# Optimization experiments

Measured on AMD Instinct MI355X. Metric: run time of the kernel, lower is better.

The kernel has to match this reference:

```python
import jax, jax.numpy as jnp
import numpy as np

N_NODES = 50000
N_REL = 8
IN_DIM = 128
HID = 128
N_EDGES = 800000
N_TRIP = 100000


def setup_inputs() -> dict:
    key = jax.random.key(0)
    ks = jax.random.split(key, 12)
    s = 0.05
    return {
        "emb": jax.random.normal(ks[0], (N_NODES, IN_DIM), jnp.float32),
        "W0": jax.random.normal(ks[1], (N_REL, IN_DIM, HID), jnp.float32) * s,
        "root0": jax.random.normal(ks[2], (IN_DIM, HID), jnp.float32) * s,
        "b0": jnp.zeros((HID,), jnp.float32),
        "W1": jax.random.normal(ks[3], (N_REL, HID, HID), jnp.float32) * s,
        "root1": jax.random.normal(ks[4], (HID, HID), jnp.float32) * s,
        "b1": jnp.zeros((HID,), jnp.float32),
        "rel_emb": jax.random.normal(ks[5], (N_REL, HID), jnp.float32),
        "edge_index": jax.random.randint(ks[6], (2, N_EDGES), 0, N_NODES, jnp.int64 if jax.config.read('jax_enable_x64') else jnp.int32),
        "edge_type": jax.random.randint(ks[7], (N_EDGES,), 0, N_REL, jnp.int32),
        "head_idx": jax.random.randint(ks[8], (N_TRIP,), 0, N_NODES, jnp.int32),
        "rel_idx": jax.random.randint(ks[9], (N_TRIP,), 0, N_REL, jnp.int32),
        "tail_idx": jax.random.randint(ks[10], (N_TRIP,), 0, N_NODES, jnp.int32),
    }


def _rgcn_layer(h, W, root, bias, src, dst, edge_type):
    # PyG RGCNConv: per-relation MEAN aggregation of neighbor features at dst,
    # transformed by the relation weight, plus root transform and bias.
    # Mean commutes with the linear map, so aggregate raw features first.
    n, r = N_NODES, N_REL
    seg = dst * r + edge_type  # (E,) joint (dst, relation) segment id
    msg = h[src]               # (E, d) irregular gather
    sums = jax.ops.segment_sum(msg, seg, num_segments=n * r)          # (N*R, d)
    cnt = jax.ops.segment_sum(jnp.ones((src.shape[0],), h.dtype), seg,
                              num_segments=n * r)                     # (N*R,)
    mean = (sums / jnp.maximum(cnt, 1.0)[:, None]).reshape(n, r, -1)  # (N, R, d)
    return jnp.einsum('nrd,rdh->nh', mean, W) + h @ root + bias


def reference(emb, W0, root0, b0, W1, root1, b1, rel_emb,
              edge_index, edge_type, head_idx, rel_idx, tail_idx):
    src = edge_index[0]
    dst = edge_index[1]
    et = edge_type.astype(jnp.int32)
    h = emb
    h = jax.nn.relu(_rgcn_layer(h, W0, root0, b0, src, dst, et))
    h = jax.nn.relu(_rgcn_layer(h, W1, root1, b1, src, dst, et))
    # DistMult score: sum(h_head * r * h_tail)
    score = jnp.sum(h[head_idx] * rel_emb[rel_idx] * h[tail_idx], axis=-1)
    return score
```

## Files before the change

kernel.cpp:

```cpp
#include <hip/hip_runtime.h>
#include <hip/hip_bf16.h>

#define N_NODES 50000
#define N_REL   8
#define DIM     128
#define N_EDGES 800000
#define N_TRIP  100000
#define NSEG    (N_NODES * N_REL)
#define NBUCKET 196
#define CAP     6144
#define CPAD    132

typedef __attribute__((ext_vector_type(8))) short bf16x8;
typedef __attribute__((ext_vector_type(4))) float f32x4;

static __device__ __forceinline__ unsigned short f2b(float f) {
    __hip_bfloat16 h = __float2bfloat16(f);
    return *reinterpret_cast<unsigned short*>(&h);
}
static __device__ __forceinline__ float blo(unsigned int u) {
    return __uint_as_float(u << 16);
}
static __device__ __forceinline__ float bhi(unsigned int u) {
    return __uint_as_float(u & 0xffff0000u);
}
static __device__ __forceinline__ int lds_off(int row, int chunk) {
    return (row * 16 + (chunk ^ (row & 7))) * 8;
}

__global__ __launch_bounds__(256) void bucket_scatter(
        const int* __restrict__ edge_index,
        const int* __restrict__ edge_type,
        int* __restrict__ gcnt,
        unsigned int* __restrict__ slack) {
    __shared__ int hist[NBUCKET];
    __shared__ int cur[NBUCKET];
    int tid = threadIdx.x;
    for (int i = tid; i < NBUCKET; i += 256) hist[i] = 0;
    __syncthreads();
    int base = blockIdx.x * 4096;
    unsigned int w[16];
    int bk[16];
    #pragma unroll
    for (int i = 0; i < 16; ++i) {
        int e = base + i * 256 + tid;
        if (e < N_EDGES) {
            int src = edge_index[e];
            int dst = edge_index[N_EDGES + e];
            int r = edge_type[e];
            w[i] = (unsigned int)src | ((unsigned int)r << 16) |
                   ((unsigned int)(dst & 255) << 19);
            bk[i] = dst >> 8;
            atomicAdd(&hist[bk[i]], 1);
        } else {
            bk[i] = -1;
        }
    }
    __syncthreads();
    for (int i = tid; i < NBUCKET; i += 256)
        cur[i] = atomicAdd(&gcnt[i], hist[i]);
    __syncthreads();
    #pragma unroll
    for (int i = 0; i < 16; ++i) {
        if (bk[i] >= 0) {
            int p = atomicAdd(&cur[bk[i]], 1);
            if (p < CAP) slack[(size_t)bk[i] * CAP + p] = w[i];
        }
    }
}

__global__ void bucket_scan(const int* __restrict__ gcnt,
                            int* __restrict__ gbase,
                            int* __restrict__ offsets) {
    __shared__ int sh[256];
    int t = threadIdx.x;
    int v = (t < NBUCKET) ? gcnt[t] : 0;
    sh[t] = v;
    __syncthreads();
    #pragma unroll
    for (int off = 1; off < 256; off <<= 1) {
        int x = (t >= off) ? sh[t - off] : 0;
        __syncthreads();
        sh[t] += x;
        __syncthreads();
    }
    if (t < NBUCKET) gbase[t] = sh[t] - v;
    if (t == 0) offsets[NSEG] = N_EDGES;
}

__global__ __launch_bounds__(256) void bucket_sort(
        const unsigned int* __restrict__ slack,
        const int* __restrict__ gcnt,
        const int* __restrict__ gbase,
        unsigned int* __restrict__ sorted_pack,
        int* __restrict__ offsets,
        float* __restrict__ invcnt) {
    __shared__ unsigned int ebuf[CAP];
    __shared__ unsigned int obuf[CAP];
    __shared__ int hist[2048];
    __shared__ int excl[2048];
    __shared__ int sh[256];
    int b = blockIdx.x, t = threadIdx.x;
    int n = gcnt[b]; if (n > CAP) n = CAP;
    int bb = gbase[b];
    for (int i = t; i < n; i += 256) ebuf[i] = slack[(size_t)b * CAP + i];
    for (int i = t; i < 2048; i += 256) hist[i] = 0;
    __syncthreads();
    for (int i = t; i < n; i += 256) {
        unsigned int w = ebuf[i];
        int seg = (int)((w >> 19) << 3) | (int)((w >> 16) & 7u);
        atomicAdd(&hist[seg], 1);
    }
    __syncthreads();
    int c[8];
    int s = 0;
    #pragma unroll
    for (int j = 0; j < 8; ++j) { c[j] = hist[t * 8 + j]; s += c[j]; }
    sh[t] = s;
    __syncthreads();
    #pragma unroll
    for (int off = 1; off < 256; off <<= 1) {
        int x = (t >= off) ? sh[t - off] : 0;
        __syncthreads();
        sh[t] += x;
        __syncthreads();
    }
    int ex = sh[t] - s;
    #pragma unroll
    for (int j = 0; j < 8; ++j) { excl[t * 8 + j] = ex; ex += c[j]; }
    __syncthreads();
    #pragma unroll
    for (int j = 0; j < 8; ++j) hist[t * 8 + j] = excl[t * 8 + j];
    __syncthreads();
    for (int i = t; i < n; i += 256) {
        unsigned int w = ebuf[i];
        int seg = (int)((w >> 19) << 3) | (int)((w >> 16) & 7u);
        int p = atomicAdd(&hist[seg], 1);
        obuf[p] = w & 0x7ffffu;
    }
    __syncthreads();
    for (int i = t; i < n; i += 256) sorted_pack[bb + i] = obuf[i];
    int segbase = b * 2048;
    #pragma unroll
    for (int j = 0; j < 8; ++j) {
        int gseg = segbase + t * 8 + j;
        if (gseg < NSEG) {
            offsets[gseg] = bb + excl[t * 8 + j];
            invcnt[gseg] = (c[j] > 0) ? 1.0f / (float)c[j] : 0.f;
        }
    }
}

__global__ void cvt_emb_kernel(const float* __restrict__ src,
                               unsigned short* __restrict__ dst) {
    int i = blockIdx.x * blockDim.x + threadIdx.x;
    const int npair = N_NODES * DIM / 2;
    if (i >= npair) return;
    float2 v = ((const float2*)src)[i];
    unsigned int p = (unsigned int)f2b(v.x) | ((unsigned int)f2b(v.y) << 16);
    ((unsigned int*)dst)[i] = p;
}

__global__ void cvt_w2_kernel(const float* __restrict__ root0,
                              const float* __restrict__ W0,
                              const float* __restrict__ root1,
                              const float* __restrict__ W1,
                              unsigned short* __restrict__ Wt2a,
                              unsigned short* __restrict__ Wt2b) {
    int s = blockIdx.x;
    int n = blockIdx.y;
    int k = threadIdx.x;
    const float* root = blockIdx.z ? root1 : root0;
    const float* W    = blockIdx.z ? W1 : W0;
    unsigned short* Wt2 = blockIdx.z ? Wt2b : Wt2a;
    float v = (s == 0) ? root[k * 128 + n]
                       : W[((size_t)(s - 1) * 128 + k) * 128 + n];
    Wt2[((size_t)s * 128 + n) * 128 + k] = f2b(v);
}

__global__ __launch_bounds__(256) void gemm9_all(
        const unsigned short* __restrict__ hb,
        const unsigned short* __restrict__ Wt2,
        unsigned short* __restrict__ Y) {
    __shared__ unsigned short Bs[128 * 16 * 8];
    __shared__ unsigned short Cs[64 * CPAD];

    int tid = threadIdx.x;
    int wave = tid >> 6, lane = tid & 63;
    int wm = wave & 1, wn = wave >> 1;
    int quad = lane >> 4, l16 = lane & 15;
    int row0 = blockIdx.x * 64;

    bf16x8 afr[2][4];
    #pragma unroll
    for (int i = 0; i < 2; ++i) {
        int grow = row0 + wm * 32 + i * 16 + l16;
        if (grow >= N_NODES) grow = N_NODES - 1;
        #pragma unroll
        for (int kk = 0; kk < 4; ++kk)
            afr[i][kk] = *(const bf16x8*)(hb + (size_t)grow * DIM + kk * 32 + quad * 8);
    }

    int er = tid >> 2, ec = (tid & 3) * 32;
    int egrow = row0 + er;
    bool estore = (egrow < N_NODES);

    for (int s = 0; s < 9; ++s) {
        __syncthreads();
        {
            int n = tid >> 1, c0 = (tid & 1) * 8;
            const unsigned short* gp = Wt2 + ((size_t)s * 128 + n) * 128 + c0 * 8;
            #pragma unroll
            for (int q = 0; q < 8; ++q)
                *(bf16x8*)&Bs[lds_off(n, c0 + q)] = *(const bf16x8*)(gp + q * 8);
        }
        __syncthreads();

        f32x4 acc[2][4];
        #pragma unroll
        for (int i = 0; i < 2; ++i)
            #pragma unroll
            for (int j = 0; j < 4; ++j) acc[i][j] = (f32x4){0.f, 0.f, 0.f, 0.f};

        #pragma unroll
        for (int kk = 0; kk < 4; ++kk) {
            int chunk = kk * 4 + quad;
            bf16x8 bfr[4];
            #pragma unroll
            for (int j = 0; j < 4; ++j)
                bfr[j] = *(const bf16x8*)&Bs[lds_off(wn * 64 + j * 16 + l16, chunk)];
            #pragma unroll
            for (int i = 0; i < 2; ++i)
                #pragma unroll
                for (int j = 0; j < 4; ++j)
                    acc[i][j] = __builtin_amdgcn_mfma_f32_16x16x32_bf16(
                        afr[i][kk], bfr[j], acc[i][j], 0, 0, 0);
        }

        #pragma unroll
        for (int i = 0; i < 2; ++i) {
            int rb = wm * 32 + i * 16 + quad * 4;
            #pragma unroll
            for (int j = 0; j < 4; ++j) {
                int col = wn * 64 + j * 16 + l16;
                #pragma unroll
                for (int r = 0; r < 4; ++r)
                    Cs[(rb + r) * CPAD + col] = f2b(acc[i][j][r]);
            }
        }
        __syncthreads();
        if (estore) {
            const uint4* cp = (const uint4*)&Cs[er * CPAD + ec];
            uint4* yp = (uint4*)(Y + ((size_t)s * N_NODES + egrow) * 128 + ec);
            uint4 v0 = cp[0], v1 = cp[1], v2 = cp[2], v3 = cp[3];
            yp[0] = v0; yp[1] = v1; yp[2] = v2; yp[3] = v3;
        }
    }
}

__global__ __launch_bounds__(256) void aggregate_out(
        const unsigned short* __restrict__ Y,
        const float* __restrict__ bias,
        const int* __restrict__ offsets,
        const unsigned int* __restrict__ sorted_pack,
        const float* __restrict__ invcnt,
        unsigned short* __restrict__ hout) {
    int dst = blockIdx.x * 4 + (threadIdx.x >> 6);
    if (dst >= N_NODES) return;
    int lane = threadIdx.x & 63;
    const unsigned int* Yu = (const unsigned int*)Y;

    unsigned int r0 = Yu[(size_t)dst * 64 + lane];
    float a0 = blo(r0), a1 = bhi(r0);

    int beg = offsets[dst * N_REL];
    int end = offsets[dst * N_REL + N_REL];
    for (int base = beg; base < end; base += 64) {
        int np = end - base; if (np > 64) np = 64;
        unsigned int pk = 0; float ivl = 0.f;
        if (lane < np) {
            pk = sorted_pack[base + lane];
            ivl = invcnt[dst * N_REL + (int)(pk >> 16)];
        }
        int j = 0;
        for (; j + 3 < np; j += 4) {
            unsigned int p0 = __shfl((int)pk, j, 64);
            unsigned int p1 = __shfl((int)pk, j + 1, 64);
            unsigned int p2 = __shfl((int)pk, j + 2, 64);
            unsigned int p3 = __shfl((int)pk, j + 3, 64);
            float i0 = __shfl(ivl, j, 64);
            float i1 = __shfl(ivl, j + 1, 64);
            float i2 = __shfl(ivl, j + 2, 64);
            float i3 = __shfl(ivl, j + 3, 64);
            unsigned int v0 = Yu[((size_t)(1 + (p0 >> 16)) * N_NODES + (p0 & 0xffffu)) * 64 + lane];
            unsigned int v1 = Yu[((size_t)(1 + (p1 >> 16)) * N_NODES + (p1 & 0xffffu)) * 64 + lane];
            unsigned int v2 = Yu[((size_t)(1 + (p2 >> 16)) * N_NODES + (p2 & 0xffffu)) * 64 + lane];
            unsigned int v3 = Yu[((size_t)(1 + (p3 >> 16)) * N_NODES + (p3 & 0xffffu)) * 64 + lane];
            a0 = fmaf(blo(v0), i0, a0); a1 = fmaf(bhi(v0), i0, a1);
            a0 = fmaf(blo(v1), i1, a0); a1 = fmaf(bhi(v1), i1, a1);
            a0 = fmaf(blo(v2), i2, a0); a1 = fmaf(bhi(v2), i2, a1);
            a0 = fmaf(blo(v3), i3, a0); a1 = fmaf(bhi(v3), i3, a1);
        }
        for (; j < np; ++j) {
            unsigned int pj = __shfl((int)pk, j, 64);
            float ij = __shfl(ivl, j, 64);
            unsigned int v = Yu[((size_t)(1 + (pj >> 16)) * N_NODES + (pj & 0xffffu)) * 64 + lane];
            a0 = fmaf(blo(v), ij, a0); a1 = fmaf(bhi(v), ij, a1);
        }
    }
    float2 bv = ((const float2*)bias)[lane];
    a0 = fmaxf(a0 + bv.x, 0.f);
    a1 = fmaxf(a1 + bv.y, 0.f);
    unsigned int po = (unsigned int)f2b(a0) | ((unsigned int)f2b(a1) << 16);
    ((unsigned int*)(hout + (size_t)dst * DIM))[lane] = po;
}

__global__ void score_kernel(const unsigned short* __restrict__ hb,
                             const float* __restrict__ rel_emb,
                             const int* __restrict__ head,
                             const int* __restrict__ rel,
                             const int* __restrict__ tail,
                             float* __restrict__ out) {
    int t = blockIdx.x * 4 + (threadIdx.x >> 6);
    if (t >= N_TRIP) return;
    int lane = threadIdx.x & 63;
    unsigned int ph = ((const unsigned int*)(hb + (size_t)head[t] * DIM))[lane];
    unsigned int pt = ((const unsigned int*)(hb + (size_t)tail[t] * DIM))[lane];
    float2 rr = ((const float2*)(rel_emb + (size_t)rel[t] * DIM))[lane];
    float s = blo(ph) * rr.x * blo(pt) + bhi(ph) * rr.y * bhi(pt);
    #pragma unroll
    for (int off = 32; off; off >>= 1) s += __shfl_xor(s, off, 64);
    if (lane == 0) out[t] = s;
}

extern "C" void kernel_launch(void* const* d_in, const int* in_sizes, int n_in,
                              void* d_out, int out_size, void* d_ws, size_t ws_size,
                              hipStream_t stream) {
    const float* emb     = (const float*)d_in[0];
    const float* W0      = (const float*)d_in[1];
    const float* root0   = (const float*)d_in[2];
    const float* b0      = (const float*)d_in[3];
    const float* W1      = (const float*)d_in[4];
    const float* root1   = (const float*)d_in[5];
    const float* b1      = (const float*)d_in[6];
    const float* rel_emb = (const float*)d_in[7];
    const int* edge_index = (const int*)d_in[8];
    const int* edge_type  = (const int*)d_in[9];
    const int* head_idx   = (const int*)d_in[10];
    const int* rel_idx    = (const int*)d_in[11];
    const int* tail_idx   = (const int*)d_in[12];
    float* out = (float*)d_out;

    char* p = (char*)d_ws;
    size_t y_bytes   = (size_t)9 * N_NODES * DIM * sizeof(unsigned short);
    size_t hb_bytes  = (size_t)N_NODES * DIM * sizeof(unsigned short);
    size_t wt2_bytes = (size_t)9 * 128 * 128 * sizeof(unsigned short);
    unsigned short* Y    = (unsigned short*)p; p += y_bytes;
    unsigned short* embb = (unsigned short*)p; p += hb_bytes;
    unsigned short* h1b  = (unsigned short*)p; p += hb_bytes;
    unsigned short* h2b  = (unsigned short*)p; p += hb_bytes;
    unsigned short* Wt2a = (unsigned short*)p; p += wt2_bytes;
    unsigned short* Wt2b = (unsigned short*)p; p += wt2_bytes;
    int* offsets = (int*)p;           p += (size_t)(NSEG + 1) * sizeof(int);
    float* invcnt = (float*)p;        p += (size_t)NSEG * sizeof(float);
    unsigned int* sorted_pack = (unsigned int*)p; p += (size_t)N_EDGES * sizeof(unsigned int);
    unsigned int* slack = (unsigned int*)p; p += (size_t)NBUCKET * CAP * sizeof(unsigned int);
    int* gcnt  = (int*)p;             p += (size_t)NBUCKET * sizeof(int);
    int* gbase = (int*)p;
    (void)ws_size; (void)in_sizes; (void)n_in; (void)out_size;

    dim3 blk256(256);

    hipMemsetAsync(gcnt, 0, (size_t)NBUCKET * sizeof(int), stream);
    bucket_scatter<<<(N_EDGES + 4095) / 4096, blk256, 0, stream>>>(edge_index, edge_type,
                                                                   gcnt, slack);
    bucket_scan<<<1, 256, 0, stream>>>(gcnt, gbase, offsets);
    bucket_sort<<<NBUCKET, blk256, 0, stream>>>(slack, gcnt, gbase, sorted_pack,
                                                offsets, invcnt);

    cvt_emb_kernel<<<(N_NODES * DIM / 2 + 255) / 256, blk256, 0, stream>>>(emb, embb);
    cvt_w2_kernel<<<dim3(9, 128, 2), 128, 0, stream>>>(root0, W0, root1, W1, Wt2a, Wt2b);

    int ggrid = (N_NODES + 63) / 64;
    int agrid = (N_NODES + 3) / 4;

    gemm9_all<<<ggrid, blk256, 0, stream>>>(embb, Wt2a, Y);
    aggregate_out<<<agrid, blk256, 0, stream>>>(Y, b0, offsets, sorted_pack, invcnt, h1b);

    gemm9_all<<<ggrid, blk256, 0, stream>>>(h1b, Wt2b, Y);
    aggregate_out<<<agrid, blk256, 0, stream>>>(Y, b1, offsets, sorted_pack, invcnt, h2b);

    score_kernel<<<(N_TRIP + 3) / 4, blk256, 0, stream>>>(h2b, rel_emb, head_idx, rel_idx,
                                                          tail_idx, out);
}
```

Measured before the change: 365.9 us.

## Remove LDS staging and barriers from per-relation GEMM, load weights directly

Rewrites the 9-slice GEMM so each wave owns 16 rows and loops over all 128 output columns. B fragments now come straight from global memory (L2-resident weights) instead of being staged through swizzled LDS. Results are stored directly as scattered 2-byte writes instead of through an LDS transpose with coalesced 16-byte stores. This removes all __syncthreads and LDS use. The cost is more global load traffic for weights and poorly coalesced output stores.

```diff
diff --git a/kernel.cpp b/kernel.cpp
--- a/kernel.cpp
+++ b/kernel.cpp
@@ -9,7 +9,6 @@
 #define NSEG    (N_NODES * N_REL)
 #define NBUCKET 196
 #define CAP     6144
-#define CPAD    132
 
 typedef __attribute__((ext_vector_type(8))) short bf16x8;
 typedef __attribute__((ext_vector_type(4))) float f32x4;
@@ -23,9 +22,6 @@
 }
 static __device__ __forceinline__ float bhi(unsigned int u) {
     return __uint_as_float(u & 0xffff0000u);
-}
-static __device__ __forceinline__ int lds_off(int row, int chunk) {
-    return (row * 16 + (chunk ^ (row & 7))) * 8;
 }
 
 __global__ __launch_bounds__(256) void bucket_scatter(
@@ -178,82 +174,48 @@
     Wt2[((size_t)s * 128 + n) * 128 + k] = f2b(v);
 }
 
-__global__ __launch_bounds__(256) void gemm9_all(
+__global__ __launch_bounds__(256) void gemm9_nobar(
         const unsigned short* __restrict__ hb,
         const unsigned short* __restrict__ Wt2,
         unsigned short* __restrict__ Y) {
-    __shared__ unsigned short Bs[128 * 16 * 8];
-    __shared__ unsigned short Cs[64 * CPAD];
-
     int tid = threadIdx.x;
     int wave = tid >> 6, lane = tid & 63;
-    int wm = wave & 1, wn = wave >> 1;
     int quad = lane >> 4, l16 = lane & 15;
-    int row0 = blockIdx.x * 64;
-
-    bf16x8 afr[2][4];
-    #pragma unroll
-    for (int i = 0; i < 2; ++i) {
-        int grow = row0 + wm * 32 + i * 16 + l16;
+    int row0 = blockIdx.x * 64 + wave * 16;
+
+    bf16x8 afr[4];
+    {
+        int grow = row0 + l16;
         if (grow >= N_NODES) grow = N_NODES - 1;
+        const unsigned short* gp = hb + (size_t)grow * DIM;
         #pragma unroll
         for (int kk = 0; kk < 4; ++kk)
-            afr[i][kk] = *(const bf16x8*)(hb + (size_t)grow * DIM + kk * 32 + quad * 8);
-    }
-
-    int er = tid >> 2, ec = (tid & 3) * 32;
-    int egrow = row0 + er;
-    bool estore = (egrow < N_NODES);
-
+            afr[kk] = *(const bf16x8*)(gp + kk * 32 + quad * 8);
+    }
+
+    int srow0 = row0 + quad * 4;
     for (int s = 0; s < 9; ++s) {
-        __syncthreads();
-        {
-            int n = tid >> 1, c0 = (tid & 1) * 8;
-            const unsigned short* gp = Wt2 + ((size_t)s * 128 + n) * 128 + c0 * 8;
-            #pragma unroll
-            for (int q = 0; q < 8; ++q)
-                *(bf16x8*)&Bs[lds_off(n, c0 + q)] = *(const bf16x8*)(gp + q * 8);
-        }
-        __syncthreads();
-
-        f32x4 acc[2][4];
+        const unsigned short* Ws = Wt2 + (size_t)s * 128 * 128;
+        unsigned short* Ys = Y + (size_t)s * N_NODES * 128;
         #pragma unroll
-        for (int i = 0; i < 2; ++i)
-            #pragma unroll
-            for (int j = 0; j < 4; ++j) acc[i][j] = (f32x4){0.f, 0.f, 0.f, 0.f};
-
-        #pragma unroll
-        for (int kk = 0; kk < 4; ++kk) {
-            int chunk = kk * 4 + quad;
+        for (int j = 0; j < 8; ++j) {
+            const unsigned short* bp = Ws + (size_t)(j * 16 + l16) * 128;
             bf16x8 bfr[4];
             #pragma unroll
-            for (int j = 0; j < 4; ++j)
-                bfr[j] = *(const bf16x8*)&Bs[lds_off(wn * 64 + j * 16 + l16, chunk)];
+            for (int kk = 0; kk < 4; ++kk)
+                bfr[kk] = *(const bf16x8*)(bp + kk * 32 + quad * 8);
+            f32x4 acc = (f32x4){0.f, 0.f, 0.f, 0.f};
             #pragma unroll
-            for (int i = 0; i < 2; ++i)
-                #pragma unroll
-                for (int j = 0; j < 4; ++j)
-                    acc[i][j] = __builtin_amdgcn_mfma_f32_16x16x32_bf16(
-                        afr[i][kk], bfr[j], acc[i][j], 0, 0, 0);
-        }
-
-        #pragma unroll
-        for (int i = 0; i < 2; ++i) {
-            int rb = wm * 32 + i * 16 + quad * 4;
+            for (int kk = 0; kk < 4; ++kk)
+                acc = __builtin_amdgcn_mfma_f32_16x16x32_bf16(
+                    afr[kk], bfr[kk], acc, 0, 0, 0);
+            int gc = j * 16 + l16;
             #pragma unroll
-            for (int j = 0; j < 4; ++j) {
-                int col = wn * 64 + j * 16 + l16;
-                #pragma unroll
-                for (int r = 0; r < 4; ++r)
-                    Cs[(rb + r) * CPAD + col] = f2b(acc[i][j][r]);
+            for (int r = 0; r < 4; ++r) {
+                int gr = srow0 + r;
+                if (gr < N_NODES)
+                    Ys[(size_t)gr * 128 + gc] = f2b(acc[r]);
             }
-        }
-        __syncthreads();
-        if (estore) {
-            const uint4* cp = (const uint4*)&Cs[er * CPAD + ec];
-            uint4* yp = (uint4*)(Y + ((size_t)s * N_NODES + egrow) * 128 + ec);
-            uint4 v0 = cp[0], v1 = cp[1], v2 = cp[2], v3 = cp[3];
-            yp[0] = v0; yp[1] = v1; yp[2] = v2; yp[3] = v3;
         }
     }
 }
@@ -384,10 +346,10 @@
     int ggrid = (N_NODES + 63) / 64;
     int agrid = (N_NODES + 3) / 4;
 
-    gemm9_all<<<ggrid, blk256, 0, stream>>>(embb, Wt2a, Y);
+    gemm9_nobar<<<ggrid, blk256, 0, stream>>>(embb, Wt2a, Y);
     aggregate_out<<<agrid, blk256, 0, stream>>>(Y, b0, offsets, sorted_pack, invcnt, h1b);
 
-    gemm9_all<<<ggrid, blk256, 0, stream>>>(h1b, Wt2b, Y);
+    gemm9_nobar<<<ggrid, blk256, 0, stream>>>(h1b, Wt2b, Y);
     aggregate_out<<<agrid, blk256, 0, stream>>>(Y, b1, offsets, sorted_pack, invcnt, h2b);
 
     score_kernel<<<(N_TRIP + 3) / 4, blk256, 0, stream>>>(h2b, rel_emb, head_idx, rel_idx,
```

After: 505.3 us. 1.38x slower.

## Load GEMM B fragments directly to registers and use per-wave epilogue staging

Applied to the files above, without the earlier changes.

The 9-slice GEMM no longer stages each weight slice in shared memory. Each wave now loads its B fragments straight from global memory (L2-resident weights) into registers. The output epilogue uses a private per-wave LDS tile instead of a block-wide tile, so all __syncthreads barriers are removed from the slice loop. This trades block barriers and LDS traffic for redundant global loads of the weights across waves, plus higher register pressure from holding 16 B fragments.

```diff
diff --git a/kernel.cpp b/kernel.cpp
--- a/kernel.cpp
+++ b/kernel.cpp
@@ -9,7 +9,7 @@
 #define NSEG    (N_NODES * N_REL)
 #define NBUCKET 196
 #define CAP     6144
-#define CPAD    132
+#define CROWS   72
 
 typedef __attribute__((ext_vector_type(8))) short bf16x8;
 typedef __attribute__((ext_vector_type(4))) float f32x4;
@@ -23,9 +23,6 @@
 }
 static __device__ __forceinline__ float bhi(unsigned int u) {
     return __uint_as_float(u & 0xffff0000u);
-}
-static __device__ __forceinline__ int lds_off(int row, int chunk) {
-    return (row * 16 + (chunk ^ (row & 7))) * 8;
 }
 
 __global__ __launch_bounds__(256) void bucket_scatter(
@@ -178,12 +175,11 @@
     Wt2[((size_t)s * 128 + n) * 128 + k] = f2b(v);
 }
 
-__global__ __launch_bounds__(256) void gemm9_all(
+__global__ __launch_bounds__(256) void gemm9_reg(
         const unsigned short* __restrict__ hb,
         const unsigned short* __restrict__ Wt2,
         unsigned short* __restrict__ Y) {
-    __shared__ unsigned short Bs[128 * 16 * 8];
-    __shared__ unsigned short Cs[64 * CPAD];
+    __shared__ unsigned short Cs[4][32 * CROWS];
 
     int tid = threadIdx.x;
     int wave = tid >> 6, lane = tid & 63;
@@ -201,20 +197,21 @@
             afr[i][kk] = *(const bf16x8*)(hb + (size_t)grow * DIM + kk * 32 + quad * 8);
     }
 
-    int er = tid >> 2, ec = (tid & 3) * 32;
-    int egrow = row0 + er;
-    bool estore = (egrow < N_NODES);
+    unsigned short* cw = &Cs[wave][0];
+    int rrow = lane >> 3, rch = lane & 7;
 
     for (int s = 0; s < 9; ++s) {
-        __syncthreads();
-        {
-            int n = tid >> 1, c0 = (tid & 1) * 8;
-            const unsigned short* gp = Wt2 + ((size_t)s * 128 + n) * 128 + c0 * 8;
+        const unsigned short* Ws = Wt2 + (size_t)s * 128 * 128;
+        unsigned short* Ys = Y + (size_t)s * N_NODES * 128;
+
+        bf16x8 bfr[4][4];
+        #pragma unroll
+        for (int j = 0; j < 4; ++j) {
+            const unsigned short* bp = Ws + (size_t)(wn * 64 + j * 16 + l16) * 128;
             #pragma unroll
-            for (int q = 0; q < 8; ++q)
-                *(bf16x8*)&Bs[lds_off(n, c0 + q)] = *(const bf16x8*)(gp + q * 8);
-        }
-        __syncthreads();
+            for (int kk = 0; kk < 4; ++kk)
+                bfr[j][kk] = *(const bf16x8*)(bp + kk * 32 + quad * 8);
+        }
 
         f32x4 acc[2][4];
         #pragma unroll
@@ -223,38 +220,33 @@
             for (int j = 0; j < 4; ++j) acc[i][j] = (f32x4){0.f, 0.f, 0.f, 0.f};
 
         #pragma unroll
-        for (int kk = 0; kk < 4; ++kk) {
-            int chunk = kk * 4 + quad;
-            bf16x8 bfr[4];
-            #pragma unroll
-            for (int j = 0; j < 4; ++j)
-                bfr[j] = *(const bf16x8*)&Bs[lds_off(wn * 64 + j * 16 + l16, chunk)];
+        for (int kk = 0; kk < 4; ++kk)
             #pragma unroll
             for (int i = 0; i < 2; ++i)
                 #pragma unroll
                 for (int j = 0; j < 4; ++j)
                     acc[i][j] = __builtin_amdgcn_mfma_f32_16x16x32_bf16(
-                        afr[i][kk], bfr[j], acc[i][j], 0, 0, 0);
-        }
-
-        #pragma unroll
-        for (int i = 0; i < 2; ++i) {
-            int rb = wm * 32 + i * 16 + quad * 4;
+                        afr[i][kk], bfr[j][kk], acc[i][j], 0, 0, 0);
+
+        #pragma unroll
+        for (int i = 0; i < 2; ++i)
             #pragma unroll
-            for (int j = 0; j < 4; ++j) {
-                int col = wn * 64 + j * 16 + l16;
+            for (int j = 0; j < 4; ++j)
                 #pragma unroll
                 for (int r = 0; r < 4; ++r)
-                    Cs[(rb + r) * CPAD + col] = f2b(acc[i][j][r]);
-            }
-        }
-        __syncthreads();
-        if (estore) {
-            const uint4* cp = (const uint4*)&Cs[er * CPAD + ec];
-            uint4* yp = (uint4*)(Y + ((size_t)s * N_NODES + egrow) * 128 + ec);
-            uint4 v0 = cp[0], v1 = cp[1], v2 = cp[2], v3 = cp[3];
-            yp[0] = v0; yp[1] = v1; yp[2] = v2; yp[3] = v3;
-        }
+                    cw[(i * 16 + quad * 4 + r) * CROWS + j * 16 + l16] =
+                        f2b(acc[i][j][r]);
+        asm volatile("" ::: "memory");
+
+        #pragma unroll
+        for (int t = 0; t < 4; ++t) {
+            int lr = t * 8 + rrow;
+            int grow = row0 + wm * 32 + lr;
+            uint4 v = *(const uint4*)&cw[lr * CROWS + rch * 8];
+            if (grow < N_NODES)
+                *(uint4*)(Ys + (size_t)grow * 128 + wn * 64 + rch * 8) = v;
+        }
+        asm volatile("" ::: "memory");
     }
 }
 
@@ -384,10 +376,10 @@
     int ggrid = (N_NODES + 63) / 64;
     int agrid = (N_NODES + 3) / 4;
 
-    gemm9_all<<<ggrid, blk256, 0, stream>>>(embb, Wt2a, Y);
+    gemm9_reg<<<ggrid, blk256, 0, stream>>>(embb, Wt2a, Y);
     aggregate_out<<<agrid, blk256, 0, stream>>>(Y, b0, offsets, sorted_pack, invcnt, h1b);
 
-    gemm9_all<<<ggrid, blk256, 0, stream>>>(h1b, Wt2b, Y);
+    gemm9_reg<<<ggrid, blk256, 0, stream>>>(h1b, Wt2b, Y);
     aggregate_out<<<agrid, blk256, 0, stream>>>(Y, b1, offsets, sorted_pack, invcnt, h2b);
 
     score_kernel<<<(N_TRIP + 3) / 4, blk256, 0, stream>>>(h2b, rel_emb, head_idx, rel_idx,
```

Result: slower. 376.3 us (+2.8%).

## Split GEMM columns across two blocks, store directly, and unroll gather by eight

Applied to the files above, without the earlier changes.

The 9-way GEMM now splits the 128 output columns into two 64-column tiles across a second grid dimension. This halves the LDS weight tile and per-wave accumulators, which should raise occupancy and parallelism. The LDS staging of the output tile is removed, so results go straight to global memory as scattered 2-byte stores, and one barrier per slice is dropped at the cost of less coalesced writes. Each column block also reloads the A fragments. Separately, the aggregation gather loop is unrolled from 4 to 8 edges so more loads are in flight.

```diff
diff --git a/kernel.cpp b/kernel.cpp
--- a/kernel.cpp
+++ b/kernel.cpp
@@ -9,7 +9,6 @@
 #define NSEG    (N_NODES * N_REL)
 #define NBUCKET 196
 #define CAP     6144
-#define CPAD    132
 
 typedef __attribute__((ext_vector_type(8))) short bf16x8;
 typedef __attribute__((ext_vector_type(4))) float f32x4;
@@ -178,18 +177,18 @@
     Wt2[((size_t)s * 128 + n) * 128 + k] = f2b(v);
 }
 
-__global__ __launch_bounds__(256) void gemm9_all(
+__global__ __launch_bounds__(256) void gemm9_bn64(
         const unsigned short* __restrict__ hb,
         const unsigned short* __restrict__ Wt2,
         unsigned short* __restrict__ Y) {
-    __shared__ unsigned short Bs[128 * 16 * 8];
-    __shared__ unsigned short Cs[64 * CPAD];
+    __shared__ unsigned short Bs[64 * 16 * 8];
 
     int tid = threadIdx.x;
     int wave = tid >> 6, lane = tid & 63;
     int wm = wave & 1, wn = wave >> 1;
     int quad = lane >> 4, l16 = lane & 15;
     int row0 = blockIdx.x * 64;
+    int col0 = blockIdx.y * 64;
 
     bf16x8 afr[2][4];
     #pragma unroll
@@ -201,59 +200,52 @@
             afr[i][kk] = *(const bf16x8*)(hb + (size_t)grow * DIM + kk * 32 + quad * 8);
     }
 
-    int er = tid >> 2, ec = (tid & 3) * 32;
-    int egrow = row0 + er;
-    bool estore = (egrow < N_NODES);
-
     for (int s = 0; s < 9; ++s) {
         __syncthreads();
         {
-            int n = tid >> 1, c0 = (tid & 1) * 8;
-            const unsigned short* gp = Wt2 + ((size_t)s * 128 + n) * 128 + c0 * 8;
-            #pragma unroll
-            for (int q = 0; q < 8; ++q)
+            int n = tid >> 2, c0 = (tid & 3) * 4;
+            const unsigned short* gp = Wt2 + ((size_t)s * 128 + col0 + n) * 128 + c0 * 8;
+            #pragma unroll
+            for (int q = 0; q < 4; ++q)
                 *(bf16x8*)&Bs[lds_off(n, c0 + q)] = *(const bf16x8*)(gp + q * 8);
         }
         __syncthreads();
 
-        f32x4 acc[2][4];
+        f32x4 acc[2][2];
         #pragma unroll
         for (int i = 0; i < 2; ++i)
             #pragma unroll
-            for (int j = 0; j < 4; ++j) acc[i][j] = (f32x4){0.f, 0.f, 0.f, 0.f};
+            for (int j = 0; j < 2; ++j) acc[i][j] = (f32x4){0.f, 0.f, 0.f, 0.f};
 
         #pragma unroll
         for (int kk = 0; kk < 4; ++kk) {
             int chunk = kk * 4 + quad;
-            bf16x8 bfr[4];
-            #pragma unroll
-            for (int j = 0; j < 4; ++j)
-                bfr[j] = *(const bf16x8*)&Bs[lds_off(wn * 64 + j * 16 + l16, chunk)];
+            bf16x8 bfr[2];
+            #pragma unroll
+            for (int j = 0; j < 2; ++j)
+                bfr[j] = *(const bf16x8*)&Bs[lds_off(wn * 32 + j * 16 + l16, chunk)];
             #pragma unroll
             for (int i = 0; i < 2; ++i)
                 #pragma unroll
-                for (int j = 0; j < 4; ++j)
+                for (int j = 0; j < 2; ++j)
                     acc[i][j] = __builtin_amdgcn_mfma_f32_16x16x32_bf16(
                         afr[i][kk], bfr[j], acc[i][j], 0, 0, 0);
         }
 
+        unsigned short* Ys = Y + (size_t)s * N_NODES * 128;
         #pragma unroll
         for (int i = 0; i < 2; ++i) {
-            int rb = wm * 32 + i * 16 + quad * 4;
-            #pragma unroll
-            for (int j = 0; j < 4; ++j) {
-                int col = wn * 64 + j * 16 + l16;
+            int gr0 = row0 + wm * 32 + i * 16 + quad * 4;
+            #pragma unroll
+            for (int j = 0; j < 2; ++j) {
+                int gc = col0 + wn * 32 + j * 16 + l16;
                 #pragma unroll
-                for (int r = 0; r < 4; ++r)
-                    Cs[(rb + r) * CPAD + col] = f2b(acc[i][j][r]);
+                for (int r = 0; r < 4; ++r) {
+                    int grow = gr0 + r;
+                    if (grow < N_NODES)
+                        Ys[(size_t)grow * 128 + gc] = f2b(acc[i][j][r]);
+                }
             }
-        }
-        __syncthreads();
-        if (estore) {
-            const uint4* cp = (const uint4*)&Cs[er * CPAD + ec];
-            uint4* yp = (uint4*)(Y + ((size_t)s * N_NODES + egrow) * 128 + ec);
-            uint4 v0 = cp[0], v1 = cp[1], v2 = cp[2], v3 = cp[3];
-            yp[0] = v0; yp[1] = v1; yp[2] = v2; yp[3] = v3;
         }
     }
 }
@@ -283,23 +275,22 @@
             ivl = invcnt[dst * N_REL + (int)(pk >> 16)];
         }
         int j = 0;
-        for (; j + 3 < np; j += 4) {
-            unsigned int p0 = __shfl((int)pk, j, 64);
-            unsigned int p1 = __shfl((int)pk, j + 1, 64);
-            unsigned int p2 = __shfl((int)pk, j + 2, 64);
-            unsigned int p3 = __shfl((int)pk, j + 3, 64);
-            float i0 = __shfl(ivl, j, 64);
-            float i1 = __shfl(ivl, j + 1, 64);
-            float i2 = __shfl(ivl, j + 2, 64);
-            float i3 = __shfl(ivl, j + 3, 64);
-            unsigned int v0 = Yu[((size_t)(1 + (p0 >> 16)) * N_NODES + (p0 & 0xffffu)) * 64 + lane];
-            unsigned int v1 = Yu[((size_t)(1 + (p1 >> 16)) * N_NODES + (p1 & 0xffffu)) * 64 + lane];
-            unsigned int v2 = Yu[((size_t)(1 + (p2 >> 16)) * N_NODES + (p2 & 0xffffu)) * 64 + lane];
-            unsigned int v3 = Yu[((size_t)(1 + (p3 >> 16)) * N_NODES + (p3 & 0xffffu)) * 64 + lane];
-            a0 = fmaf(blo(v0), i0, a0); a1 = fmaf(bhi(v0), i0, a1);
-            a0 = fmaf(blo(v1), i1, a0); a1 = fmaf(bhi(v1), i1, a1);
-            a0 = fmaf(blo(v2), i2, a0); a1 = fmaf(bhi(v2), i2, a1);
-            a0 = fmaf(blo(v3), i3, a0); a1 = fmaf(bhi(v3), i3, a1);
+        for (; j + 7 < np; j += 8) {
+            unsigned int pp[8]; float ii[8];
+            #pragma unroll
+            for (int q = 0; q < 8; ++q) {
+                pp[q] = __shfl((int)pk, j + q, 64);
+                ii[q] = __shfl(ivl, j + q, 64);
+            }
+            unsigned int vv[8];
+            #pragma unroll
+            for (int q = 0; q < 8; ++q)
+                vv[q] = Yu[((size_t)(1 + (pp[q] >> 16)) * N_NODES + (pp[q] & 0xffffu)) * 64 + lane];
+            #pragma unroll
+            for (int q = 0; q < 8; ++q) {
+                a0 = fmaf(blo(vv[q]), ii[q], a0);
+                a1 = fmaf(bhi(vv[q]), ii[q], a1);
+            }
         }
         for (; j < np; ++j) {
             unsigned int pj = __shfl((int)pk, j, 64);
@@ -381,13 +372,13 @@
     cvt_emb_kernel<<<(N_NODES * DIM / 2 + 255) / 256, blk256, 0, stream>>>(emb, embb);
     cvt_w2_kernel<<<dim3(9, 128, 2), 128, 0, stream>>>(root0, W0, root1, W1, Wt2a, Wt2b);
 
-    int ggrid = (N_NODES + 63) / 64;
+    dim3 ggrid((N_NODES + 63) / 64, 2);
     int agrid = (N_NODES + 3) / 4;
 
-    gemm9_all<<<ggrid, blk256, 0, stream>>>(embb, Wt2a, Y);
+    gemm9_bn64<<<ggrid, blk256, 0, stream>>>(embb, Wt2a, Y);
     aggregate_out<<<agrid, blk256, 0, stream>>>(Y, b0, offsets, sorted_pack, invcnt, h1b);
 
-    gemm9_all<<<ggrid, blk256, 0, stream>>>(h1b, Wt2b, Y);
+    gemm9_bn64<<<ggrid, blk256, 0, stream>>>(h1b, Wt2b, Y);
     aggregate_out<<<agrid, blk256, 0, stream>>>(Y, b1, offsets, sorted_pack, invcnt, h2b);
 
     score_kernel<<<(N_TRIP + 3) / 4, blk256, 0, stream>>>(h2b, rel_emb, head_idx, rel_idx,
```

New measurement: 328.4 us. 1.11x faster.
